# Kernel tuning notes

Measured on AMD Instinct MI355X. Metric: run time of the kernel, lower is better.

## Reference

```python
import jax, jax.numpy as jnp
import numpy as np

CH = 64          # channels
OC = 64          # out_channels
B, H, W = 8, 128, 128
NCA_C = CH + OC  # 128, NCA state channels
K = 3            # kernel_size
DILS = (1, 2, 4, 8)
HID = 64         # NCA update hidden
EPS = 1e-5


def setup_inputs() -> dict:
    key = jax.random.key(0)
    ks = jax.random.split(key, 16)
    def n(k, shape, s=0.02):
        return jax.random.normal(k, shape, jnp.float32) * s
    return {
        "x": jax.random.normal(ks[0], (B, H, W, CH), jnp.float32),
        "c": jax.random.normal(ks[1], (B, OC), jnp.float32),
        # Attention params
        "Wq": n(ks[2], (CH, OC)), "bq": jnp.zeros((OC,), jnp.float32),
        "Wk": n(ks[3], (OC, OC)), "bk": jnp.zeros((OC,), jnp.float32),
        "Wv": n(ks[4], (OC, OC)), "bv": jnp.zeros((OC,), jnp.float32),
        "Wo": n(ks[5], (OC, OC)), "bo": jnp.zeros((OC,), jnp.float32),
        "ln_g": jnp.ones((OC,), jnp.float32), "ln_b": jnp.zeros((OC,), jnp.float32),
        # NCA depthwise perception kernels, one per dilation: [4, NCA_C, 1, K, K]
        "pk": n(ks[6], (len(DILS), NCA_C, 1, K, K), 0.1),
        # NCA update MLP
        "W1": n(ks[7], ((1 + len(DILS)) * NCA_C, HID)), "b1": jnp.zeros((HID,), jnp.float32),
        "W2": n(ks[8], (HID, CH)), "b2": jnp.zeros((CH,), jnp.float32),
    }


def _layernorm(z, g, b):
    m = jnp.mean(z, axis=-1, keepdims=True)
    v = jnp.var(z, axis=-1, keepdims=True)
    return (z - m) / jnp.sqrt(v + EPS) * g + b


def _forward(x, c, Wq, bq, Wk, bk, Wv, bv, Wo, bo, ln_g, ln_b, pk, W1, b1, W2, b2):
    b_, h_, w_, _ = x.shape
    # ---- Attention(x, c): single-key softmax pooling over H*W ----
    q = x.reshape(b_, h_ * w_, CH) @ Wq + bq              # [B, HW, OC]
    k = c @ Wk + bk                                        # [B, OC]
    v = c @ Wv + bv                                        # [B, OC]
    scores = jnp.einsum('bno,bo->bn', q, k) * (OC ** -0.5)  # [B, HW]
    attn = jax.nn.softmax(scores, axis=1)                  # softmax over spatial dim
    attended = jnp.einsum('bn,bo->bo', attn, v)            # weighted pool (weights sum to 1)
    a = _layernorm(attended @ Wo + bo + c, ln_g, ln_b)     # out_proj + residual + LN
    c2 = c + a                                             # outer residual in NCAAttention

    # ---- concat broadcast context -> NCA state [B,H,W,NCA_C] ----
    c_exp = jnp.broadcast_to(c2[:, None, None, :], (b_, h_, w_, OC))
    xc = jnp.concatenate([x, c_exp], axis=-1)

    # ---- NCA perception: depthwise dilated convs (SAME padding) ----
    xp = jnp.transpose(xc, (0, 3, 1, 2))                   # NCHW
    feats = [xc]
    for i, d in enumerate(DILS):
        pad = d * (K // 2)
        p = jax.lax.conv_general_dilated(
            xp, pk[i], window_strides=(1, 1),
            padding=[(pad, pad), (pad, pad)], rhs_dilation=(d, d),
            dimension_numbers=('NCHW', 'OIHW', 'NCHW'),
            feature_group_count=NCA_C)
        feats.append(jnp.transpose(p, (0, 2, 3, 1)))
    upd_in = jnp.concatenate(feats, axis=-1)               # [B,H,W,5*NCA_C]

    # ---- NCA update MLP: Linear -> (Dropout=id) -> GELU -> Linear ----
    hidden = jax.nn.gelu(upd_in @ W1 + b1, approximate=False)
    y = hidden @ W2 + b2                                   # [B,H,W,CH]
    # NCA.out_channels (64) != NCA.channels (128) -> no residual add
    return y, c2


def reference(x, c, Wq, bq, Wk, bk, Wv, bv, Wo, bo, ln_g, ln_b, pk, W1, b1, W2, b2):
    return _forward(x, c, Wq, bq, Wk, bk, Wv, bv, Wo, bo, ln_g, ln_b, pk, W1, b1, W2, b2)
```

## Files before the change

kernel.cpp:

```cpp
#include <hip/hip_runtime.h>
#include <hip/hip_bf16.h>
#include <math.h>


typedef float  f32x4 __attribute__((ext_vector_type(4)));
typedef short  s16x8 __attribute__((ext_vector_type(8)));
typedef long   i64x2 __attribute__((ext_vector_type(2)));

static __device__ __forceinline__ unsigned short f2bf(float f) {
    __hip_bfloat16 h = __float2bfloat16(f);
    unsigned short u; __builtin_memcpy(&u, &h, 2); return u;
}
static __device__ __forceinline__ unsigned pk4fp8(float f0, float f1, float f2, float f3) {
    int v = 0;
    v = __builtin_amdgcn_cvt_pk_fp8_f32(f0, f1, v, false);
    v = __builtin_amdgcn_cvt_pk_fp8_f32(f2, f3, v, true);
    return (unsigned)v;
}

#define XROWB  9216
#define XBATCH 1327104
#define USCALE 256.0f

__global__ void prep2(const float* __restrict__ x,  const float* __restrict__ pk,
                      const float* __restrict__ W1, const float* __restrict__ W2,
                      const float* __restrict__ b1,
                      const float* __restrict__ c,
                      const float* __restrict__ Wv, const float* __restrict__ bv,
                      const float* __restrict__ Wo, const float* __restrict__ bo,
                      const float* __restrict__ lng, const float* __restrict__ lnb,
                      unsigned char* __restrict__ xp, unsigned char* __restrict__ Uf,
                      unsigned short* __restrict__ W2s,
                      float* __restrict__ V, float* __restrict__ hcp,
                      float* __restrict__ outc2)
{
    const int blk = blockIdx.x, tid = threadIdx.x;
    __shared__ float sc[512], sv[512], c2s[512];

    if (blk >= 683) {
        sc[tid] = c[tid]; sc[tid + 256] = c[tid + 256];
        __syncthreads();
        #pragma unroll
        for (int half = 0; half < 2; ++half) {
            int it = tid + half*256;
            int bb = it >> 6, j = it & 63;
            float v = bv[j];
            for (int i = 0; i < 64; ++i) v += sc[bb*64 + i]*Wv[i*64 + j];
            sv[it] = v;
        }
        __syncthreads();
        #pragma unroll
        for (int half = 0; half < 2; ++half) {
            int it = tid + half*256;
            int bb = it >> 6, j = it & 63;
            float t = bo[j] + sc[it];
            for (int i = 0; i < 64; ++i) t += sv[bb*64 + i]*Wo[i*64 + j];
            float s = t;
            for (int o = 32; o > 0; o >>= 1) s += __shfl_xor(s, o);
            float m = s * (1.f/64.f);
            float dq = (t - m)*(t - m);
            for (int o = 32; o > 0; o >>= 1) dq += __shfl_xor(dq, o);
            float a = (t - m) / sqrtf(dq*(1.f/64.f) + 1e-5f) * lng[j] + lnb[j];
            c2s[it] = sc[it] + a;
        }
        __syncthreads();
    }

    if (blk < 512) {
        int i = blk*256 + tid;
        int xc = i & 127, y = (i >> 7) & 127, b = i >> 14;
        const float* src = x + (size_t)i*64;
        float4 f[16];
        #pragma unroll
        for (int k = 0; k < 16; ++k) f[k] = *(const float4*)(src + k*4);
        unsigned P[16];
        #pragma unroll
        for (int k = 0; k < 16; ++k) P[k] = pk4fp8(f[k].x, f[k].y, f[k].z, f[k].w);
        unsigned char* d = xp + (size_t)b*XBATCH + (size_t)(y+8)*XROWB + (size_t)(xc+8)*64;
        *(uint4*)(d +  0) = make_uint4(P[0], P[1], P[8],  P[9]);
        *(uint4*)(d + 16) = make_uint4(P[2], P[3], P[10], P[11]);
        *(uint4*)(d + 32) = make_uint4(P[4], P[5], P[12], P[13]);
        *(uint4*)(d + 48) = make_uint4(P[6], P[7], P[14], P[15]);
    } else if (blk < 648) {
        int idx = (blk - 512)*256 + tid;
        int b = idx / 4352, r = idx - b*4352;
        int yy, xx;
        if (r < 2304) { int ry = r / 144; xx = r - ry*144; yy = (ry < 8) ? ry : 128 + ry; }
        else { int r2 = r - 2304; yy = 8 + (r2 >> 4); int xi = r2 & 15; xx = (xi < 8) ? xi : 128 + xi; }
        unsigned char* d = xp + (size_t)b*XBATCH + (size_t)yy*XROWB + (size_t)xx*64;
        uint4 z = make_uint4(0,0,0,0);
        *(uint4*)(d) = z; *(uint4*)(d+16) = z; *(uint4*)(d+32) = z; *(uint4*)(d+48) = z;
    } else if (blk < 681) {
        int idx = (blk - 648)*256 + tid;
        if (idx < 8448) {
            int lane = idx & 63, nt = (idx >> 6) & 3, pos = idx >> 8;
            int n  = nt*16 + (lane & 15);
            static constexpr int DI[33] = {3,3,3, 2,2,2, 1,1,1, 0,0,0, -1, 0,0, 1,1, 2,2, 3,3,
                                           0,0,0, 1,1,1, 2,2,2, 3,3,3};
            static constexpr int TT[33] = {0,1,2, 0,1,2, 0,1,2, 0,1,2, 4, 3,5, 3,5, 3,5, 3,5,
                                           6,7,8, 6,7,8, 6,7,8, 6,7,8};
            int di = DI[pos], t = TT[pos];
            float vv[16];
            #pragma unroll
            for (int kc2 = 0; kc2 < 2; ++kc2)
                #pragma unroll
                for (int j = 0; j < 8; ++j) {
                    int ch = kc2*32 + (lane >> 4)*8 + j;
                    float v;
                    if (di < 0) {
                        v = W1[ch*64 + n];
                        for (int dd = 0; dd < 4; ++dd)
                            v += pk[(dd*128 + ch)*9 + 4] * W1[((1+dd)*128 + ch)*64 + n];
                    } else {
                        v = pk[(di*128 + ch)*9 + t] * W1[((1+di)*128 + ch)*64 + n];
                    }
                    vv[kc2*8 + j] = v * USCALE;
                }
            uint4 o;
            o.x = pk4fp8(vv[0],  vv[1],  vv[2],  vv[3]);
            o.y = pk4fp8(vv[4],  vv[5],  vv[6],  vv[7]);
            o.z = pk4fp8(vv[8],  vv[9],  vv[10], vv[11]);
            o.w = pk4fp8(vv[12], vv[13], vv[14], vv[15]);
            *(uint4*)(Uf + (size_t)idx*16) = o;
        }
    } else if (blk < 683) {
        int idx = (blk - 681)*256 + tid;
        int lane = idx & 63, nt = (idx >> 6) & 3, kc2 = (idx >> 8) & 1;
        int n  = nt*16 + (lane & 15);
        int k0 = kc2*32 + (lane >> 4)*8;
        unsigned short e[8];
        #pragma unroll
        for (int j = 0; j < 8; ++j) e[j] = f2bf(W2[(k0+j)*64 + n]);
        uint4 o;
        o.x = (unsigned)e[0] | ((unsigned)e[1] << 16);
        o.y = (unsigned)e[2] | ((unsigned)e[3] << 16);
        o.z = (unsigned)e[4] | ((unsigned)e[5] << 16);
        o.w = (unsigned)e[6] | ((unsigned)e[7] << 16);
        *(uint4*)(W2s + (size_t)idx*8) = o;
    } else if (blk < 755) {
        int idx = (blk - 683)*256 + tid;
        int n = idx & 63, q = idx >> 6;
        int p = q % 36, b = q / 36;
        int di = p/9, t = p%9;
        float s = 0.f;
        for (int j = 0; j < 64; ++j)
            s += c2s[b*64 + j] * pk[(di*128 + 64 + j)*9 + t] * W1[((1+di)*128 + 64 + j)*64 + n];
        V[(size_t)q*64 + n] = s;
    } else {
        for (int it = tid; it < 512; it += 256) {
            int b = it >> 6, n = it & 63;
            float s = b1[n];
            for (int j = 0; j < 64; ++j) s += c2s[b*64 + j]*W1[(64 + j)*64 + n];
            hcp[it] = s;
            if (blk == 755) outc2[it] = c2s[it];
        }
    }
}

#define HID_S 72

__global__ __launch_bounds__(256, 4) void nca_main(
    const unsigned char* __restrict__ xp,
    const unsigned char* __restrict__ U,
    const unsigned short* __restrict__ W2s,
    const float* __restrict__ V,
    const float* __restrict__ hcp,
    const float* __restrict__ b2,
    float* __restrict__ out)
{
    __shared__ unsigned short hid[128*HID_S];
    __shared__ float V_l[36*64];
    __shared__ float Cx_l[16*64];
    __shared__ float Cy_l[64];
    __shared__ float hc2_l[64];

    const int tid = threadIdx.x;
    const int blk = blockIdx.x;
    const int b  = blk & 7;
    const int y  = blk >> 3;

    {
        const float4* Vg = (const float4*)(V + (size_t)b*2304);
        for (int i = tid; i < 576; i += 256) ((float4*)V_l)[i] = Vg[i];
    }
    __syncthreads();
    for (int it = tid; it < 1024; it += 256) {
        int xi = it >> 6, n = it & 63;
        int xx = xi < 8 ? xi : 112 + xi;
        float s = 0.f;
        #pragma unroll
        for (int di = 0; di < 4; ++di) {
            int d = 1 << di;
            int dxo = (xx < d) ? 0 : ((xx >= 128 - d) ? 2 : -1);
            if (dxo >= 0) {
                s += V_l[(di*9 + 0*3 + dxo)*64 + n];
                s += V_l[(di*9 + 1*3 + dxo)*64 + n];
                s += V_l[(di*9 + 2*3 + dxo)*64 + n];
            }
        }
        Cx_l[it] = s;
    }
    if (tid < 64) {
        int n = tid;
        float s = 0.f;
        #pragma unroll
        for (int di = 0; di < 4; ++di) {
            int d = 1 << di;
            int dyo = (y < d) ? 0 : ((y >= 128 - d) ? 2 : -1);
            if (dyo >= 0) {
                s += V_l[(di*9 + dyo*3 + 0)*64 + n];
                s += V_l[(di*9 + dyo*3 + 1)*64 + n];
                s += V_l[(di*9 + dyo*3 + 2)*64 + n];
            }
        }
        Cy_l[n] = s;
    } else if (tid < 128) {
        int n = tid - 64;
        float s = hcp[b*64 + n];
        for (int p = 0; p < 36; ++p) s += V_l[p*64 + n];
        hc2_l[n] = s;
    }
    __syncthreads();

    const int lane = tid & 63;
    const int w    = tid >> 6;
    const int xw   = w * 32;
    const int ln15 = lane & 15;
    const int oct  = lane >> 4;

    const unsigned char* abase = xp + (size_t)b*XBATCH + (size_t)(y + 8)*XROWB
                               + (size_t)(xw + ln15 + 8)*64 + oct*16;
    const unsigned char* ubase = U + (size_t)lane*16;

    f32x4 acc[2][4];
    #pragma unroll
    for (int mt = 0; mt < 2; ++mt)
        #pragma unroll
        for (int nt = 0; nt < 4; ++nt) {
            acc[mt][nt][0] = 0.f; acc[mt][nt][1] = 0.f;
            acc[mt][nt][2] = 0.f; acc[mt][nt][3] = 0.f;
        }

    static constexpr int OFF[33] = {
        (-8*144-8)*64, (-8*144)*64, (-8*144+8)*64,
        (-4*144-4)*64, (-4*144)*64, (-4*144+4)*64,
        (-2*144-2)*64, (-2*144)*64, (-2*144+2)*64,
        (-1*144-1)*64, (-1*144)*64, (-1*144+1)*64,
        0,
        -64, 64, -128, 128, -256, 256, -512, 512,
        ( 1*144-1)*64, ( 1*144)*64, ( 1*144+1)*64,
        ( 2*144-2)*64, ( 2*144)*64, ( 2*144+2)*64,
        ( 4*144-4)*64, ( 4*144)*64, ( 4*144+4)*64,
        ( 8*144-8)*64, ( 8*144)*64, ( 8*144+8)*64
    };

    auto load_AB = [&](int pos, i64x2* A, i64x2* Bv) {
        const unsigned char* rp = abase + OFF[pos];
        #pragma unroll
        for (int mt = 0; mt < 2; ++mt) A[mt] = *(const i64x2*)(rp + mt*1024);
        const unsigned char* up = ubase + (size_t)pos*4096;
        #pragma unroll
        for (int nt = 0; nt < 4; ++nt) Bv[nt] = *(const i64x2*)(up + nt*1024);
    };
    auto mfma_step = [&](const i64x2* A, const i64x2* Bv) {
        #pragma unroll
        for (int kc2 = 0; kc2 < 2; ++kc2)
            #pragma unroll
            for (int nt = 0; nt < 4; ++nt) {
                long bf = Bv[nt][kc2];
                #pragma unroll
                for (int mt = 0; mt < 2; ++mt)
                    acc[mt][nt] = __builtin_amdgcn_mfma_f32_16x16x32_fp8_fp8(A[mt][kc2], bf, acc[mt][nt], 0, 0, 0);
            }
    };

    i64x2 A0[2], A1[2], B0[4], B1[4];
    load_AB(0, A0, B0);
    #pragma unroll 1
    for (int it2 = 0; it2 < 16; ++it2) {
        load_AB(2*it2 + 1, A1, B1);
        mfma_step(A0, B0);
        load_AB(2*it2 + 2, A0, B0);
        mfma_step(A1, B1);
    }
    mfma_step(A0, B0);

    const bool yedge = (y < 8) || (y >= 120);
    #pragma unroll
    for (int mt = 0; mt < 2; ++mt) {
        #pragma unroll
        for (int nt = 0; nt < 4; ++nt) {
            const int n = nt*16 + ln15;
            const float hcv = hc2_l[n];
            const float cyv = yedge ? Cy_l[n] : 0.f;
            #pragma unroll
            for (int r = 0; r < 4; ++r) {
                int m = oct*4 + r;
                int x = xw + mt*16 + m;
                float h = acc[mt][nt][r]*(1.0f/USCALE) + hcv - cyv;
                if (x < 8 || x >= 120) {
                    int xi = (x < 8) ? x : (x - 112);
                    h -= Cx_l[xi*64 + n];
                    if (yedge) {
                        #pragma unroll
                        for (int di = 0; di < 4; ++di) {
                            int d = 1 << di;
                            int dyo = (y < d) ? 0 : ((y >= 128 - d) ? 2 : -1);
                            int dxo = (x < d) ? 0 : ((x >= 128 - d) ? 2 : -1);
                            if (dyo >= 0 && dxo >= 0)
                                h += V_l[(di*9 + dyo*3 + dxo)*64 + n];
                        }
                    }
                }
                float u = 0.7978845608028654f * (h + 0.044715f*h*h*h);
                float g = h / (1.f + __expf(-2.f*u));
                hid[x*HID_S + n] = f2bf(g);
            }
        }
    }

    f32x4 acc2[2][4];
    #pragma unroll
    for (int mt = 0; mt < 2; ++mt)
        #pragma unroll
        for (int nt = 0; nt < 4; ++nt) {
            acc2[mt][nt][0] = 0.f; acc2[mt][nt][1] = 0.f;
            acc2[mt][nt][2] = 0.f; acc2[mt][nt][3] = 0.f;
        }
    #pragma unroll
    for (int kc2 = 0; kc2 < 2; ++kc2) {
        s16x8 a2[2];
        #pragma unroll
        for (int mt = 0; mt < 2; ++mt)
            a2[mt] = *(const s16x8*)&hid[(xw + mt*16 + ln15)*HID_S + kc2*32 + oct*8];
        #pragma unroll
        for (int nt = 0; nt < 4; ++nt) {
            s16x8 bf = *(const s16x8*)(W2s + ((size_t)(kc2*4 + nt)*64 + lane)*8);
            #pragma unroll
            for (int mt = 0; mt < 2; ++mt)
                acc2[mt][nt] = __builtin_amdgcn_mfma_f32_16x16x32_bf16(a2[mt], bf, acc2[mt][nt], 0, 0, 0);
        }
    }

    float* ob = out + ((size_t)(b*128 + y))*128*64;
    #pragma unroll
    for (int nt = 0; nt < 4; ++nt) {
        const float b2v = b2[nt*16 + ln15];
        #pragma unroll
        for (int mt = 0; mt < 2; ++mt) {
            #pragma unroll
            for (int r = 0; r < 4; ++r) {
                int x = xw + mt*16 + oct*4 + r;
                ob[(size_t)x*64 + nt*16 + ln15] = acc2[mt][nt][r] + b2v;
            }
        }
    }
}

extern "C" void kernel_launch(void* const* d_in, const int* in_sizes, int n_in,
                              void* d_out, int out_size, void* d_ws, size_t ws_size,
                              hipStream_t stream) {
    const float* x   = (const float*)d_in[0];
    const float* c   = (const float*)d_in[1];
    const float* Wv  = (const float*)d_in[6];
    const float* bv  = (const float*)d_in[7];
    const float* Wo  = (const float*)d_in[8];
    const float* bo  = (const float*)d_in[9];
    const float* lng = (const float*)d_in[10];
    const float* lnb = (const float*)d_in[11];
    const float* pk  = (const float*)d_in[12];
    const float* W1  = (const float*)d_in[13];
    const float* b1  = (const float*)d_in[14];
    const float* W2  = (const float*)d_in[15];
    const float* b2  = (const float*)d_in[16];
    float* out = (float*)d_out;

    char* w = (char*)d_ws;
    unsigned char*  xpb = (unsigned char*)(w);
    unsigned char*  Uf  = (unsigned char*)(w + 10616832);
    unsigned short* W2s = (unsigned short*)(w + 10752000);
    float*          V   = (float*)         (w + 10760192);
    float*          hcp = (float*)         (w + 10833920);

    prep2<<<757, 256, 0, stream>>>(x, pk, W1, W2, b1, c, Wv, bv, Wo, bo, lng, lnb,
                                   xpb, Uf, W2s, V, hcp, out + 8388608);
    nca_main<<<1024, 256, 0, stream>>>(xpb, Uf, W2s, V, hcp, b2, out);
}
```

Baseline: 166.7 us.

## Stage fp8 weight tiles in LDS via async double-buffered loads, two rows per block

```diff
diff --git a/kernel.cpp b/kernel.cpp
--- a/kernel.cpp
+++ b/kernel.cpp
@@ -159,7 +159,7 @@
 
 #define HID_S 72
 
-__global__ __launch_bounds__(256, 4) void nca_main(
+__global__ __launch_bounds__(512, 4) void nca_main(
     const unsigned char* __restrict__ xp,
     const unsigned char* __restrict__ U,
     const unsigned short* __restrict__ W2s,
@@ -168,23 +168,34 @@
     const float* __restrict__ b2,
     float* __restrict__ out)
 {
-    __shared__ unsigned short hid[128*HID_S];
+    __shared__ __align__(16) unsigned char smem[36864];
     __shared__ float V_l[36*64];
     __shared__ float Cx_l[16*64];
-    __shared__ float Cy_l[64];
+    __shared__ float Cy_l[2*64];
     __shared__ float hc2_l[64];
+
+    unsigned short* hid = (unsigned short*)smem;
 
     const int tid = threadIdx.x;
     const int blk = blockIdx.x;
     const int b  = blk & 7;
-    const int y  = blk >> 3;
+    const int y0 = (blk >> 3) * 2;
+
+    #pragma unroll
+    for (int s = 0; s < 2; ++s) {
+        int off = tid*16 + s*8192;
+        __builtin_amdgcn_global_load_lds(
+            (const __attribute__((address_space(1))) unsigned int*)(U + off),
+            (__attribute__((address_space(3))) unsigned int*)(smem + off),
+            16, 0, 0);
+    }
 
     {
         const float4* Vg = (const float4*)(V + (size_t)b*2304);
-        for (int i = tid; i < 576; i += 256) ((float4*)V_l)[i] = Vg[i];
+        for (int i = tid; i < 576; i += 512) ((float4*)V_l)[i] = Vg[i];
     }
     __syncthreads();
-    for (int it = tid; it < 1024; it += 256) {
+    for (int it = tid; it < 1024; it += 512) {
         int xi = it >> 6, n = it & 63;
         int xx = xi < 8 ? xi : 112 + xi;
         float s = 0.f;
@@ -200,22 +211,23 @@
         }
         Cx_l[it] = s;
     }
-    if (tid < 64) {
-        int n = tid;
+    if (tid < 128) {
+        int r = tid >> 6, n = tid & 63;
+        int yy = y0 + r;
         float s = 0.f;
         #pragma unroll
         for (int di = 0; di < 4; ++di) {
             int d = 1 << di;
-            int dyo = (y < d) ? 0 : ((y >= 128 - d) ? 2 : -1);
+            int dyo = (yy < d) ? 0 : ((yy >= 128 - d) ? 2 : -1);
             if (dyo >= 0) {
                 s += V_l[(di*9 + dyo*3 + 0)*64 + n];
                 s += V_l[(di*9 + dyo*3 + 1)*64 + n];
                 s += V_l[(di*9 + dyo*3 + 2)*64 + n];
             }
         }
-        Cy_l[n] = s;
-    } else if (tid < 128) {
-        int n = tid - 64;
+        Cy_l[tid] = s;
+    } else if (tid < 192) {
+        int n = tid - 128;
         float s = hcp[b*64 + n];
         for (int p = 0; p < 36; ++p) s += V_l[p*64 + n];
         hc2_l[n] = s;
@@ -224,13 +236,14 @@
 
     const int lane = tid & 63;
     const int w    = tid >> 6;
-    const int xw   = w * 32;
+    const int rib  = w >> 2;
+    const int y    = y0 + rib;
+    const int xw   = (w & 3) * 32;
     const int ln15 = lane & 15;
     const int oct  = lane >> 4;
 
     const unsigned char* abase = xp + (size_t)b*XBATCH + (size_t)(y + 8)*XROWB
                                + (size_t)(xw + ln15 + 8)*64 + oct*16;
-    const unsigned char* ubase = U + (size_t)lane*16;
 
     f32x4 acc[2][4];
     #pragma unroll
@@ -254,36 +267,63 @@
         ( 8*144-8)*64, ( 8*144)*64, ( 8*144+8)*64
     };
 
-    auto load_AB = [&](int pos, i64x2* A, i64x2* Bv) {
+    auto loadA = [&](int pos, i64x2* A) {
         const unsigned char* rp = abase + OFF[pos];
-        #pragma unroll
-        for (int mt = 0; mt < 2; ++mt) A[mt] = *(const i64x2*)(rp + mt*1024);
-        const unsigned char* up = ubase + (size_t)pos*4096;
-        #pragma unroll
-        for (int nt = 0; nt < 4; ++nt) Bv[nt] = *(const i64x2*)(up + nt*1024);
+        A[0] = *(const i64x2*)(rp);
+        A[1] = *(const i64x2*)(rp + 1024);
+    };
+    auto loadB = [&](int bufofs, int p, i64x2* Bv) {
+        const unsigned char* rp = smem + bufofs + p*4096 + lane*16;
+        #pragma unroll
+        for (int nt = 0; nt < 4; ++nt) Bv[nt] = *(const i64x2*)(rp + nt*1024);
     };
     auto mfma_step = [&](const i64x2* A, const i64x2* Bv) {
         #pragma unroll
         for (int kc2 = 0; kc2 < 2; ++kc2)
             #pragma unroll
             for (int nt = 0; nt < 4; ++nt) {
-                long bf = Bv[nt][kc2];
+                long bfr = Bv[nt][kc2];
                 #pragma unroll
                 for (int mt = 0; mt < 2; ++mt)
-                    acc[mt][nt] = __builtin_amdgcn_mfma_f32_16x16x32_fp8_fp8(A[mt][kc2], bf, acc[mt][nt], 0, 0, 0);
+                    acc[mt][nt] = __builtin_amdgcn_mfma_f32_16x16x32_fp8_fp8(A[mt][kc2], bfr, acc[mt][nt], 0, 0, 0);
             }
     };
 
-    i64x2 A0[2], A1[2], B0[4], B1[4];
-    load_AB(0, A0, B0);
+    i64x2 Areg[2][2], Breg[2][4];
+    loadA(0, Areg[0]);
+    loadB(0, 0, Breg[0]);
+
+    int cur = 0;
     #pragma unroll 1
-    for (int it2 = 0; it2 < 16; ++it2) {
-        load_AB(2*it2 + 1, A1, B1);
-        mfma_step(A0, B0);
-        load_AB(2*it2 + 2, A0, B0);
-        mfma_step(A1, B1);
-    }
-    mfma_step(A0, B0);
+    for (int kb = 0; kb < 8; ++kb) {
+        {
+            const int nbytes = (kb < 7) ? 16384 : 4096;
+            const unsigned char* gsrc = U + (size_t)(kb + 1)*16384;
+            unsigned char* ldst = smem + (cur ^ 1)*16384;
+            for (int off = tid*16; off < nbytes; off += 8192)
+                __builtin_amdgcn_global_load_lds(
+                    (const __attribute__((address_space(1))) unsigned int*)(gsrc + off),
+                    (__attribute__((address_space(3))) unsigned int*)(ldst + off),
+                    16, 0, 0);
+        }
+        const int cofs = cur*16384;
+        #pragma unroll
+        for (int p = 0; p < 4; ++p) {
+            const int pos = kb*4 + p;
+            loadA(pos + 1, Areg[(p + 1) & 1]);
+            if (p < 3) loadB(cofs, p + 1, Breg[(p + 1) & 1]);
+            __builtin_amdgcn_s_setprio(1);
+            mfma_step(Areg[p & 1], Breg[p & 1]);
+            __builtin_amdgcn_s_setprio(0);
+        }
+        __syncthreads();
+        cur ^= 1;
+        loadB(cur*16384, 0, Breg[0]);
+    }
+    __builtin_amdgcn_s_setprio(1);
+    mfma_step(Areg[0], Breg[0]);
+    __builtin_amdgcn_s_setprio(0);
+    __syncthreads();
 
     const bool yedge = (y < 8) || (y >= 120);
     #pragma unroll
@@ -292,7 +332,7 @@
         for (int nt = 0; nt < 4; ++nt) {
             const int n = nt*16 + ln15;
             const float hcv = hc2_l[n];
-            const float cyv = yedge ? Cy_l[n] : 0.f;
+            const float cyv = yedge ? Cy_l[rib*64 + n] : 0.f;
             #pragma unroll
             for (int r = 0; r < 4; ++r) {
                 int m = oct*4 + r;
@@ -314,7 +354,7 @@
                 }
                 float u = 0.7978845608028654f * (h + 0.044715f*h*h*h);
                 float g = h / (1.f + __expf(-2.f*u));
-                hid[x*HID_S + n] = f2bf(g);
+                hid[(rib*128 + x)*HID_S + n] = f2bf(g);
             }
         }
     }
@@ -332,13 +372,13 @@
         s16x8 a2[2];
         #pragma unroll
         for (int mt = 0; mt < 2; ++mt)
-            a2[mt] = *(const s16x8*)&hid[(xw + mt*16 + ln15)*HID_S + kc2*32 + oct*8];
+            a2[mt] = *(const s16x8*)&hid[(rib*128 + xw + mt*16 + ln15)*HID_S + kc2*32 + oct*8];
         #pragma unroll
         for (int nt = 0; nt < 4; ++nt) {
-            s16x8 bf = *(const s16x8*)(W2s + ((size_t)(kc2*4 + nt)*64 + lane)*8);
+            s16x8 bfr = *(const s16x8*)(W2s + ((size_t)(kc2*4 + nt)*64 + lane)*8);
             #pragma unroll
             for (int mt = 0; mt < 2; ++mt)
-                acc2[mt][nt] = __builtin_amdgcn_mfma_f32_16x16x32_bf16(a2[mt], bf, acc2[mt][nt], 0, 0, 0);
+                acc2[mt][nt] = __builtin_amdgcn_mfma_f32_16x16x32_bf16(a2[mt], bfr, acc2[mt][nt], 0, 0, 0);
         }
     }
 
@@ -384,5 +424,5 @@
 
     prep2<<<757, 256, 0, stream>>>(x, pk, W1, W2, b1, c, Wv, bv, Wo, bo, lng, lnb,
                                    xpb, Uf, W2s, V, hcp, out + 8388608);
-    nca_main<<<1024, 256, 0, stream>>>(xpb, Uf, W2s, V, hcp, b2, out);
+    nca_main<<<512, 512, 0, stream>>>(xpb, Uf, W2s, V, hcp, b2, out);
 }
```

Result: faster. 154.5 us (-7.3%).
